# Kernel optimization log

Measured on AMD Instinct MI355X. Metric: run time of the kernel, lower is better.

Reference implementation:

```python
import jax, jax.numpy as jnp
import numpy as np

H, QP, VP, D, DP = 4, 4, 4, 128, 64
DH = D // H


def setup_inputs() -> dict:
    key = jax.random.key(0)
    ks = jax.random.split(key, 16)
    B, L = 1, 1024
    w_c0 = float(np.log(np.e - 1.0))
    inp = {
        'single': jax.random.normal(ks[0], (B, L, D), jnp.float32),
        'pair': jax.random.normal(ks[1], (B, L, L, DP), jnp.float32),
        'T': jax.random.normal(ks[2], (B, L, 4, 4), jnp.float32),
        'w_C': jnp.full((H,), w_c0, jnp.float32),
        'ln_g': jnp.ones((D,), jnp.float32),
        'ln_b': jnp.zeros((D,), jnp.float32),
        'Wq': jax.random.normal(ks[3], (D, H * DH), jnp.float32) * 0.05,
        'Wk': jax.random.normal(ks[4], (D, H * DH), jnp.float32) * 0.05,
        'Wv': jax.random.normal(ks[5], (D, H * DH), jnp.float32) * 0.05,
        'Wqpt': jax.random.normal(ks[6], (D, H * QP * 3), jnp.float32) * 0.05,
        'Wkpt': jax.random.normal(ks[7], (D, H * QP * 3), jnp.float32) * 0.05,
        'Wvpt': jax.random.normal(ks[8], (D, H * VP * 3), jnp.float32) * 0.05,
        'Wb': jax.random.normal(ks[9], (DP, H), jnp.float32) * 0.05,
        'Wout': jax.random.normal(ks[10], (H * (DH + DP + VP * 3 + VP), D), jnp.float32) * 0.05,
        'b_out': jnp.zeros((D,), jnp.float32),
    }
    return inp


def _layernorm(x, g, b, eps=1e-5):
    x32 = x.astype(jnp.float32)
    mu = x32.mean(-1, keepdims=True)
    var = ((x32 - mu) ** 2).mean(-1, keepdims=True)
    return ((x32 - mu) * jax.lax.rsqrt(var + eps) * g + b).astype(x.dtype)


def reference(single, pair, T, w_C, ln_g, ln_b, Wq, Wk, Wv, Wqpt, Wkpt, Wvpt, Wb, Wout, b_out):
    B, L, Dm = single.shape
    scale_attn = DH ** (-0.5)
    z = _layernorm(single, ln_g, ln_b)
    Q = (z @ Wq).reshape(B, L, H, DH)
    K = (z @ Wk).reshape(B, L, H, DH)
    V = (z @ Wv).reshape(B, L, H, DH)
    Q_pt = (z @ Wqpt).reshape(B, L, H, QP, 3)
    K_pt = (z @ Wkpt).reshape(B, L, H, QP, 3)
    V_pt = (z @ Wvpt).reshape(B, L, H, VP, 3)
    R = T[..., :3, :3]   # [B,L,3,3]
    t = T[..., :3, 3]    # [B,L,3]
    # global-frame points: R @ p + t
    Q_g = jnp.einsum('blxy,blhpy->blhpx', R, Q_pt) + t[:, :, None, None, :]
    K_g = jnp.einsum('blxy,blhpy->blhpx', R, K_pt) + t[:, :, None, None, :]
    V_g = jnp.einsum('blxy,blhpy->blhpx', R, V_pt) + t[:, :, None, None, :]
    # scalar QK score [B,H,L,L]
    s_attn = jnp.einsum('bihd,bjhd->bhij', Q, K) * scale_attn
    # pair bias [B,H,L,L]
    b_attn = jnp.einsum('bijc,ch->bhij', pair, Wb)
    # squared point distance [B,H,L,L]
    diff = Q_g[:, :, None] - K_g[:, None]          # [B,L,L,H,QP,3]
    d2 = jnp.moveaxis((diff ** 2).sum((-1, -2)), -1, 1)
    w_pt = jax.nn.softplus(w_C)[None, :, None, None]
    attn = jax.nn.softmax(s_attn + b_attn - 0.5 * w_pt * d2, axis=-1)
    # scalar values [B,L,H*DH]
    o_s = jnp.einsum('bhij,bjhd->bihd', attn, V).reshape(B, L, H * DH)
    # point values aggregated in global frame then mapped back: R^T (p - t)
    o_pt_g = jnp.einsum('bhij,bjhpx->bihpx', attn, V_g)
    o_pt = jnp.einsum('blyx,blhpy->blhpx', R, o_pt_g - t[:, :, None, None, :])
    o_pt_n = jnp.sqrt((o_pt ** 2).sum(-1))
    # pair aggregation [B,L,H*DP]
    o_pair = jnp.einsum('bhij,bijc->bihc', attn, pair).reshape(B, L, H * DP)
    out = jnp.concatenate([o_s, o_pair, o_pt.reshape(B, L, -1), o_pt_n.reshape(B, L, -1)], axis=-1)
    return single + out @ Wout + b_out
```

## Files before the change

kernel.cpp:

```cpp
#include <hip/hip_runtime.h>
#include <math.h>

#define L_SEQ 1024
#define DM 128
#define JC 64
#define NCHUNK (L_SEQ / JC)

#define OFF_KHAT 0
#define OFF_QHAT (L_SEQ * 192)
#define OFF_V    (OFF_QHAT + L_SEQ * 192)
#define OFF_VG   (OFF_V + L_SEQ * DM)

__global__ __launch_bounds__(256) void ipa_prep(
    const float* __restrict__ single, const float* __restrict__ T,
    const float* __restrict__ w_C, const float* __restrict__ ln_g, const float* __restrict__ ln_b,
    const float* __restrict__ Wq, const float* __restrict__ Wk, const float* __restrict__ Wv,
    const float* __restrict__ Wqpt, const float* __restrict__ Wkpt, const float* __restrict__ Wvpt,
    float* __restrict__ ws)
{
    __shared__ float z_lds[4][128];
    __shared__ float proj[4][528];
    __shared__ float qg[4][4][4][3];
    __shared__ float kg[4][4][4][3];
    __shared__ float cq[4][4], ck[4][4];

    const int t = threadIdx.x;
    const int wv = t >> 6, lane = t & 63;
    const int i0 = blockIdx.x << 2;
    const int i = i0 + wv;

    float x0 = single[i*DM + lane];
    float x1 = single[i*DM + 64 + lane];
    float s = x0 + x1, s2 = x0*x0 + x1*x1;
    #pragma unroll
    for (int off = 1; off < 64; off <<= 1) { s += __shfl_xor(s, off); s2 += __shfl_xor(s2, off); }
    float mu = s * 0.0078125f;
    float var = s2 * 0.0078125f - mu*mu;
    float rs = rsqrtf(var + 1e-5f);
    z_lds[wv][lane]      = (x0 - mu) * rs * ln_g[lane]      + ln_b[lane];
    z_lds[wv][lane + 64] = (x1 - mu) * rs * ln_g[lane + 64] + ln_b[lane + 64];
    __syncthreads();

    for (int cc = t; cc < 528; cc += 256) {
        const float* W; int col, ncol;
        if (cc < 128)      { W = Wq;   col = cc;       ncol = 128; }
        else if (cc < 256) { W = Wk;   col = cc - 128; ncol = 128; }
        else if (cc < 384) { W = Wv;   col = cc - 256; ncol = 128; }
        else if (cc < 432) { W = Wqpt; col = cc - 384; ncol = 48;  }
        else if (cc < 480) { W = Wkpt; col = cc - 432; ncol = 48;  }
        else               { W = Wvpt; col = cc - 480; ncol = 48;  }
        float a0 = 0.f, a1 = 0.f, a2 = 0.f, a3 = 0.f;
        #pragma unroll 8
        for (int k = 0; k < 128; ++k) {
            float w = W[k*ncol + col];
            a0 = fmaf(z_lds[0][k], w, a0);
            a1 = fmaf(z_lds[1][k], w, a1);
            a2 = fmaf(z_lds[2][k], w, a2);
            a3 = fmaf(z_lds[3][k], w, a3);
        }
        proj[0][cc] = a0; proj[1][cc] = a1; proj[2][cc] = a2; proj[3][cc] = a3;
    }
    __syncthreads();

    if (t < 64) {
        int r = t >> 4, h = (t >> 2) & 3, p = t & 3;
        int ii = i0 + r;
        float R[3][3], tt[3];
        #pragma unroll
        for (int x = 0; x < 3; ++x) {
            #pragma unroll
            for (int y = 0; y < 3; ++y) R[x][y] = T[ii*16 + x*4 + y];
            tt[x] = T[ii*16 + x*4 + 3];
        }
        int base = 384 + (h*4 + p)*3;
        float q0 = proj[r][base],    q1 = proj[r][base+1],  q2 = proj[r][base+2];
        float k0 = proj[r][base+48], k1 = proj[r][base+49], k2 = proj[r][base+50];
        float v0 = proj[r][base+96], v1 = proj[r][base+97], v2 = proj[r][base+98];
        #pragma unroll
        for (int x = 0; x < 3; ++x) {
            float qq = R[x][0]*q0 + R[x][1]*q1 + R[x][2]*q2 + tt[x];
            float kk = R[x][0]*k0 + R[x][1]*k1 + R[x][2]*k2 + tt[x];
            float vv = R[x][0]*v0 + R[x][1]*v1 + R[x][2]*v2 + tt[x];
            qg[r][h][p][x] = qq;
            kg[r][h][p][x] = kk;
            ws[OFF_VG + ii*48 + h*12 + p*3 + x] = vv;
        }
    }
    __syncthreads();

    if (t < 32) {
        int r = t >> 3, h = (t >> 1) & 3, isk = t & 1;
        float w = w_C[h];
        float wp = log1pf(__expf(w));
        float sq = 0.f;
        #pragma unroll
        for (int p = 0; p < 4; ++p)
            #pragma unroll
            for (int x = 0; x < 3; ++x) {
                float g = isk ? kg[r][h][p][x] : qg[r][h][p][x];
                sq += g*g;
            }
        float c = -0.5f * wp * sq;
        if (isk) ck[r][h] = c; else cq[r][h] = c;
    }
    __syncthreads();

    for (int idx = t; idx < 512; idx += 256) {
        int r = idx >> 7, d = idx & 127;
        ws[OFF_V + (size_t)(i0 + r)*DM + d] = proj[r][256 + d];
    }
    const float scale_attn = 0.17677669529663687f;
    for (int idx = t; idx < 768; idx += 256) {
        int r = idx / 192, rem = idx % 192;
        int h = rem / 48, k = rem % 48;
        int ii = i0 + r;
        float w = w_C[h];
        float wp = log1pf(__expf(w));
        float kv, qv;
        if (k < 32) {
            kv = proj[r][128 + h*32 + k];
            qv = scale_attn * proj[r][h*32 + k];
        } else if (k < 44) {
            int e = k - 32;
            kv = kg[r][h][e/3][e%3];
            qv = wp * qg[r][h][e/3][e%3];
        } else if (k == 44) { kv = ck[r][h]; qv = 1.0f; }
        else if (k == 45)   { kv = 1.0f;    qv = cq[r][h]; }
        else                { kv = 0.f;     qv = 0.f; }
        ws[OFF_KHAT + (size_t)ii*192 + h*48 + k] = kv;
        ws[OFF_QHAT + (size_t)ii*192 + h*48 + k] = qv;
    }
}

__global__ __launch_bounds__(256, 2) void ipa_attn(
    const float* __restrict__ single, const float* __restrict__ pair,
    const float* __restrict__ T, const float* __restrict__ Wb,
    const float* __restrict__ Wout, const float* __restrict__ b_out,
    const float* __restrict__ ws, float* __restrict__ out)
{
    __shared__ __align__(16) float4 pair_lds[2][JC][16];
    __shared__ float bias_part[4][2][JC][5];
    __shared__ float p_lds[4][2][JC];
    __shared__ float alpha_lds[4][2];
    __shared__ float l_lds[4][2];
    __shared__ __align__(16) float4 qhat_lds[2][4][12];
    __shared__ __align__(16) float4 wb_lds[64];
    __shared__ float og_lds[2][4][12];
    __shared__ __align__(16) float u_lds[2][448];

    const int t = threadIdx.x;
    const int wv = t >> 6, lane = t & 63;
    const int i0 = blockIdx.x * 2;

    if (t < 96)       ((float4*)qhat_lds)[t] = ((const float4*)(ws + OFF_QHAT))[(size_t)i0*48 + t];
    else if (t < 160) wb_lds[t - 96] = ((const float4*)Wb)[t - 96];

    float m0 = -INFINITY, m1 = -INFINITY, l0 = 0.f, l1 = 0.f;
    float4 accp[2][4];
    float4 accs[2];
    float4 accg[2];
    #pragma unroll
    for (int r = 0; r < 2; ++r) {
        accs[r] = make_float4(0.f,0.f,0.f,0.f);
        accg[r] = make_float4(0.f,0.f,0.f,0.f);
        #pragma unroll
        for (int h = 0; h < 4; ++h) accp[r][h] = make_float4(0.f,0.f,0.f,0.f);
    }

    const float4* pair4 = (const float4*)pair;
    const float4* kh4   = (const float4*)(ws + OFF_KHAT);
    const float4* v4    = (const float4*)(ws + OFF_V);
    const float4* vg4   = (const float4*)(ws + OFF_VG);

    __syncthreads();

    for (int ch = 0; ch < NCHUNK; ++ch) {
        const int j0 = ch * JC;
        #pragma unroll
        for (int it = 0; it < 8; ++it) {
            int idx = t + 256*it;
            int c4 = idx & 15, rj = idx >> 4;
            int row = rj >> 6, j = rj & 63;
            float4 pv = pair4[((size_t)(i0 + row)*L_SEQ + j0 + j)*16 + c4];
            pair_lds[row][j][c4 ^ (j & 7)] = pv;
        }
        __syncthreads();

        {
            float b00=0,b01=0,b02=0,b03=0, b10=0,b11=0,b12=0,b13=0;
            #pragma unroll
            for (int c4p = 0; c4p < 4; ++c4p) {
                int c4 = (wv << 2) + c4p;
                float4 w0 = wb_lds[c4*4+0], w1 = wb_lds[c4*4+1], w2 = wb_lds[c4*4+2], w3 = wb_lds[c4*4+3];
                int sw = c4 ^ (lane & 7);
                float4 p0 = pair_lds[0][lane][sw];
                float4 p1 = pair_lds[1][lane][sw];
                b00 += p0.x*w0.x + p0.y*w1.x + p0.z*w2.x + p0.w*w3.x;
                b01 += p0.x*w0.y + p0.y*w1.y + p0.z*w2.y + p0.w*w3.y;
                b02 += p0.x*w0.z + p0.y*w1.z + p0.z*w2.z + p0.w*w3.z;
                b03 += p0.x*w0.w + p0.y*w1.w + p0.z*w2.w + p0.w*w3.w;
                b10 += p1.x*w0.x + p1.y*w1.x + p1.z*w2.x + p1.w*w3.x;
                b11 += p1.x*w0.y + p1.y*w1.y + p1.z*w2.y + p1.w*w3.y;
                b12 += p1.x*w0.z + p1.y*w1.z + p1.z*w2.z + p1.w*w3.z;
                b13 += p1.x*w0.w + p1.y*w1.w + p1.z*w2.w + p1.w*w3.w;
            }
            bias_part[wv][0][lane][0]=b00; bias_part[wv][0][lane][1]=b01;
            bias_part[wv][0][lane][2]=b02; bias_part[wv][0][lane][3]=b03;
            bias_part[wv][1][lane][0]=b10; bias_part[wv][1][lane][1]=b11;
            bias_part[wv][1][lane][2]=b12; bias_part[wv][1][lane][3]=b13;
        }
        __syncthreads();

        {
            float4 kh[12];
            const float4* kp = kh4 + (size_t)(j0 + lane)*48 + wv*12;
            #pragma unroll
            for (int k4 = 0; k4 < 12; ++k4) kh[k4] = kp[k4];
            #pragma unroll
            for (int row = 0; row < 2; ++row) {
                float d = 0.f;
                #pragma unroll
                for (int k4 = 0; k4 < 12; ++k4) {
                    float4 q = qhat_lds[row][wv][k4];
                    d = fmaf(kh[k4].x, q.x, d); d = fmaf(kh[k4].y, q.y, d);
                    d = fmaf(kh[k4].z, q.z, d); d = fmaf(kh[k4].w, q.w, d);
                }
                float bias = bias_part[0][row][lane][wv] + bias_part[1][row][lane][wv]
                           + bias_part[2][row][lane][wv] + bias_part[3][row][lane][wv];
                float logit = d + bias;
                float cmax = logit;
                #pragma unroll
                for (int off = 1; off < 64; off <<= 1) cmax = fmaxf(cmax, __shfl_xor(cmax, off));
                float mo = row ? m1 : m0;
                float mn = fmaxf(mo, cmax);
                float alpha = __expf(mo - mn);
                float p = __expf(logit - mn);
                float ps = p;
                #pragma unroll
                for (int off = 1; off < 64; off <<= 1) ps += __shfl_xor(ps, off);
                if (row) { l1 = l1*alpha + ps; m1 = mn; } else { l0 = l0*alpha + ps; m0 = mn; }
                p_lds[wv][row][lane] = p;
                if (lane == 0) alpha_lds[wv][row] = alpha;
            }
        }
        __syncthreads();

        {
            float al[4][2];
            #pragma unroll
            for (int h = 0; h < 4; ++h) { al[h][0] = alpha_lds[h][0]; al[h][1] = alpha_lds[h][1]; }
            #pragma unroll
            for (int r = 0; r < 2; ++r) {
                #pragma unroll
                for (int h = 0; h < 4; ++h) {
                    float a = al[h][r];
                    accp[r][h].x *= a; accp[r][h].y *= a; accp[r][h].z *= a; accp[r][h].w *= a;
                }
                float a = al[wv][r];
                accs[r].x *= a; accs[r].y *= a; accs[r].z *= a; accs[r].w *= a;
                accg[r].x *= a; accg[r].y *= a; accg[r].z *= a; accg[r].w *= a;
            }
            {
                int c4p = lane & 3, jg = lane >> 2;
                #pragma unroll
                for (int jj = 0; jj < 4; ++jj) {
                    int j = jg + 16*jj;
                    int sw = ((wv << 2) + c4p) ^ (j & 7);
                    #pragma unroll
                    for (int r = 0; r < 2; ++r) {
                        float4 pv = pair_lds[r][j][sw];
                        float pw0 = p_lds[0][r][j], pw1 = p_lds[1][r][j];
                        float pw2 = p_lds[2][r][j], pw3 = p_lds[3][r][j];
                        accp[r][0].x = fmaf(pw0, pv.x, accp[r][0].x); accp[r][0].y = fmaf(pw0, pv.y, accp[r][0].y);
                        accp[r][0].z = fmaf(pw0, pv.z, accp[r][0].z); accp[r][0].w = fmaf(pw0, pv.w, accp[r][0].w);
                        accp[r][1].x = fmaf(pw1, pv.x, accp[r][1].x); accp[r][1].y = fmaf(pw1, pv.y, accp[r][1].y);
                        accp[r][1].z = fmaf(pw1, pv.z, accp[r][1].z); accp[r][1].w = fmaf(pw1, pv.w, accp[r][1].w);
                        accp[r][2].x = fmaf(pw2, pv.x, accp[r][2].x); accp[r][2].y = fmaf(pw2, pv.y, accp[r][2].y);
                        accp[r][2].z = fmaf(pw2, pv.z, accp[r][2].z); accp[r][2].w = fmaf(pw2, pv.w, accp[r][2].w);
                        accp[r][3].x = fmaf(pw3, pv.x, accp[r][3].x); accp[r][3].y = fmaf(pw3, pv.y, accp[r][3].y);
                        accp[r][3].z = fmaf(pw3, pv.z, accp[r][3].z); accp[r][3].w = fmaf(pw3, pv.w, accp[r][3].w);
                    }
                }
            }
            {
                int d4 = lane & 7, jg = lane >> 3;
                #pragma unroll
                for (int jj = 0; jj < 8; ++jj) {
                    int j = jg + 8*jj;
                    float4 vv = v4[(size_t)(j0 + j)*32 + wv*8 + d4];
                    float pa = p_lds[wv][0][j], pb = p_lds[wv][1][j];
                    accs[0].x = fmaf(pa, vv.x, accs[0].x); accs[0].y = fmaf(pa, vv.y, accs[0].y);
                    accs[0].z = fmaf(pa, vv.z, accs[0].z); accs[0].w = fmaf(pa, vv.w, accs[0].w);
                    accs[1].x = fmaf(pb, vv.x, accs[1].x); accs[1].y = fmaf(pb, vv.y, accs[1].y);
                    accs[1].z = fmaf(pb, vv.z, accs[1].z); accs[1].w = fmaf(pb, vv.w, accs[1].w);
                }
            }
            {
                int g4 = lane & 3, jg = lane >> 2;
                #pragma unroll
                for (int jj = 0; jj < 4; ++jj) {
                    int j = jg + 16*jj;
                    float4 gv = make_float4(0.f,0.f,0.f,0.f);
                    if (g4 < 3) gv = vg4[(size_t)(j0 + j)*12 + wv*3 + g4];
                    float pa = p_lds[wv][0][j], pb = p_lds[wv][1][j];
                    accg[0].x = fmaf(pa, gv.x, accg[0].x); accg[0].y = fmaf(pa, gv.y, accg[0].y);
                    accg[0].z = fmaf(pa, gv.z, accg[0].z); accg[0].w = fmaf(pa, gv.w, accg[0].w);
                    accg[1].x = fmaf(pb, gv.x, accg[1].x); accg[1].y = fmaf(pb, gv.y, accg[1].y);
                    accg[1].z = fmaf(pb, gv.z, accg[1].z); accg[1].w = fmaf(pb, gv.w, accg[1].w);
                }
            }
        }
        __syncthreads();
    }

    #pragma unroll
    for (int r = 0; r < 2; ++r) {
        #pragma unroll
        for (int h = 0; h < 4; ++h) {
            #pragma unroll
            for (int off = 4; off < 64; off <<= 1) {
                accp[r][h].x += __shfl_xor(accp[r][h].x, off);
                accp[r][h].y += __shfl_xor(accp[r][h].y, off);
                accp[r][h].z += __shfl_xor(accp[r][h].z, off);
                accp[r][h].w += __shfl_xor(accp[r][h].w, off);
            }
        }
        #pragma unroll
        for (int off = 8; off < 64; off <<= 1) {
            accs[r].x += __shfl_xor(accs[r].x, off); accs[r].y += __shfl_xor(accs[r].y, off);
            accs[r].z += __shfl_xor(accs[r].z, off); accs[r].w += __shfl_xor(accs[r].w, off);
        }
        #pragma unroll
        for (int off = 4; off < 64; off <<= 1) {
            accg[r].x += __shfl_xor(accg[r].x, off); accg[r].y += __shfl_xor(accg[r].y, off);
            accg[r].z += __shfl_xor(accg[r].z, off); accg[r].w += __shfl_xor(accg[r].w, off);
        }
    }
    if (lane == 0) { l_lds[wv][0] = l0; l_lds[wv][1] = l1; }
    __syncthreads();
    float invl[4][2];
    #pragma unroll
    for (int h = 0; h < 4; ++h) { invl[h][0] = 1.f / l_lds[h][0]; invl[h][1] = 1.f / l_lds[h][1]; }

    if (lane < 8) {
        #pragma unroll
        for (int r = 0; r < 2; ++r) {
            float sc = invl[wv][r];
            int base = wv*32 + lane*4;
            u_lds[r][base+0] = accs[r].x*sc; u_lds[r][base+1] = accs[r].y*sc;
            u_lds[r][base+2] = accs[r].z*sc; u_lds[r][base+3] = accs[r].w*sc;
        }
    }
    if (lane < 4) {
        #pragma unroll
        for (int r = 0; r < 2; ++r)
            #pragma unroll
            for (int h = 0; h < 4; ++h) {
                float sc = invl[h][r];
                int base = 128 + h*64 + wv*16 + lane*4;
                u_lds[r][base+0] = accp[r][h].x*sc; u_lds[r][base+1] = accp[r][h].y*sc;
                u_lds[r][base+2] = accp[r][h].z*sc; u_lds[r][base+3] = accp[r][h].w*sc;
            }
    }
    if (lane < 3) {
        #pragma unroll
        for (int r = 0; r < 2; ++r) {
            float sc = invl[wv][r];
            og_lds[r][wv][lane*4+0] = accg[r].x*sc; og_lds[r][wv][lane*4+1] = accg[r].y*sc;
            og_lds[r][wv][lane*4+2] = accg[r].z*sc; og_lds[r][wv][lane*4+3] = accg[r].w*sc;
        }
    }
    __syncthreads();

    if (t < 32) {
        int r = t >> 4, idx = t & 15, h = idx >> 2, p = idx & 3;
        int ii = i0 + r;
        float R[3][3], tt[3];
        #pragma unroll
        for (int x = 0; x < 3; ++x) {
            #pragma unroll
            for (int y = 0; y < 3; ++y) R[x][y] = T[ii*16 + x*4 + y];
            tt[x] = T[ii*16 + x*4 + 3];
        }
        float v0 = og_lds[r][h][p*3+0] - tt[0];
        float v1 = og_lds[r][h][p*3+1] - tt[1];
        float v2 = og_lds[r][h][p*3+2] - tt[2];
        float n2 = 0.f;
        #pragma unroll
        for (int x = 0; x < 3; ++x) {
            float o = R[0][x]*v0 + R[1][x]*v1 + R[2][x]*v2;
            u_lds[r][384 + h*12 + p*3 + x] = o;
            n2 += o*o;
        }
        u_lds[r][432 + h*4 + p] = sqrtf(n2);
    }
    __syncthreads();

    {
        int r = t >> 7, d = t & 127;
        int ii = i0 + r;
        float acc = single[ii*DM + d] + b_out[d];
        const float4* u4 = (const float4*)u_lds[r];
        #pragma unroll 4
        for (int k4 = 0; k4 < 112; ++k4) {
            float4 u = u4[k4];
            const float* wp = Wout + (size_t)(k4*4)*128 + d;
            acc = fmaf(u.x, wp[0],   acc);
            acc = fmaf(u.y, wp[128], acc);
            acc = fmaf(u.z, wp[256], acc);
            acc = fmaf(u.w, wp[384], acc);
        }
        out[ii*DM + d] = acc;
    }
}

extern "C" void kernel_launch(void* const* d_in, const int* in_sizes, int n_in,
                              void* d_out, int out_size, void* d_ws, size_t ws_size,
                              hipStream_t stream)
{
    const float* single = (const float*)d_in[0];
    const float* pair   = (const float*)d_in[1];
    const float* T      = (const float*)d_in[2];
    const float* w_C    = (const float*)d_in[3];
    const float* ln_g   = (const float*)d_in[4];
    const float* ln_b   = (const float*)d_in[5];
    const float* Wq     = (const float*)d_in[6];
    const float* Wk     = (const float*)d_in[7];
    const float* Wv     = (const float*)d_in[8];
    const float* Wqpt   = (const float*)d_in[9];
    const float* Wkpt   = (const float*)d_in[10];
    const float* Wvpt   = (const float*)d_in[11];
    const float* Wb     = (const float*)d_in[12];
    const float* Wout   = (const float*)d_in[13];
    const float* b_out  = (const float*)d_in[14];
    float* out = (float*)d_out;
    float* ws  = (float*)d_ws;

    ipa_prep<<<256, 256, 0, stream>>>(single, T, w_C, ln_g, ln_b, Wq, Wk, Wv, Wqpt, Wkpt, Wvpt, ws);
    ipa_attn<<<512, 256, 0, stream>>>(single, pair, T, Wb, Wout, b_out, ws, out);
}
```

Baseline: 494.4 us.

## Double-buffer pair tiles with async global-to-LDS loads and halve chunk size

Pair tiles are now loaded straight into LDS with global_load_lds into a two-slot buffer, so the next chunk's fetch overlaps compute on the current one. The chunk size drops from 64 to 32 keys, and each wave now handles both query rows at once with a remapped lane layout for the bias, softmax and accumulation stages. K-hat, V and VG loads are hoisted ahead of the bias stage to hide their latency. In exchange there are twice as many chunk iterations, barriers written in inline asm with hand-set vmcnt waits, and different reduction lane patterns that must match exactly.

Measured after the change: 473.8 us. 4.2% less time.

```diff
diff --git a/kernel.cpp b/kernel.cpp
--- a/kernel.cpp
+++ b/kernel.cpp
@@ -3,13 +3,21 @@
 
 #define L_SEQ 1024
 #define DM 128
-#define JC 64
-#define NCHUNK (L_SEQ / JC)
+#define JC 32
+#define NCH (L_SEQ / JC)
 
 #define OFF_KHAT 0
 #define OFF_QHAT (L_SEQ * 192)
 #define OFF_V    (OFF_QHAT + L_SEQ * 192)
 #define OFF_VG   (OFF_V + L_SEQ * DM)
+
+typedef __attribute__((address_space(1))) const void* gas_t;
+typedef __attribute__((address_space(3))) void* las_t;
+
+__device__ __forceinline__ void async16(const float4* g, float4* l) {
+    __builtin_amdgcn_global_load_lds((gas_t)g, (las_t)l, 16, 0, 0);
+}
+#define ASYNC_BAR() asm volatile("s_waitcnt lgkmcnt(0)\n\ts_barrier" ::: "memory")
 
 __global__ __launch_bounds__(256) void ipa_prep(
     const float* __restrict__ single, const float* __restrict__ T,
@@ -138,7 +146,7 @@
     const float* __restrict__ Wout, const float* __restrict__ b_out,
     const float* __restrict__ ws, float* __restrict__ out)
 {
-    __shared__ __align__(16) float4 pair_lds[2][JC][16];
+    __shared__ __align__(16) float4 pair_lds[2][2][JC][16];
     __shared__ float bias_part[4][2][JC][5];
     __shared__ float p_lds[4][2][JC];
     __shared__ float alpha_lds[4][2];
@@ -155,7 +163,14 @@
     if (t < 96)       ((float4*)qhat_lds)[t] = ((const float4*)(ws + OFF_QHAT))[(size_t)i0*48 + t];
     else if (t < 160) wb_lds[t - 96] = ((const float4*)Wb)[t - 96];
 
-    float m0 = -INFINITY, m1 = -INFINITY, l0 = 0.f, l1 = 0.f;
+    const int r_b = lane >> 5, j_b = lane & 31;
+    const int r_s = lane & 1,  j_s = lane >> 1;
+    const int d4  = lane & 7,  jg_s = lane >> 3;
+    const int c4p = lane >> 4, jg_p = lane & 15;
+    const int g4  = lane & 3,  jg_g = lane >> 2;
+    const int g4c = (g4 < 3) ? g4 : 0;
+
+    float m_run = -INFINITY, l_run = 0.f;
     float4 accp[2][4];
     float4 accs[2];
     float4 accg[2];
@@ -171,79 +186,98 @@
     const float4* kh4   = (const float4*)(ws + OFF_KHAT);
     const float4* v4    = (const float4*)(ws + OFF_V);
     const float4* vg4   = (const float4*)(ws + OFF_VG);
-
-    __syncthreads();
-
-    for (int ch = 0; ch < NCHUNK; ++ch) {
+    float4* plds_flat   = &pair_lds[0][0][0][0];
+
+    {
+        #pragma unroll
+        for (int it = 0; it < 4; ++it) {
+            int idx = it*256 + t;
+            int row = idx >> 9, j = (idx >> 4) & 31, slot = idx & 15;
+            int c4 = slot ^ (j & 7);
+            async16(pair4 + ((size_t)(i0 + row)*L_SEQ + j)*16 + c4, plds_flat + idx);
+        }
+    }
+
+    for (int ch = 0; ch < NCH; ++ch) {
+        const int cur = ch & 1;
         const int j0 = ch * JC;
-        #pragma unroll
-        for (int it = 0; it < 8; ++it) {
-            int idx = t + 256*it;
-            int c4 = idx & 15, rj = idx >> 4;
-            int row = rj >> 6, j = rj & 63;
-            float4 pv = pair4[((size_t)(i0 + row)*L_SEQ + j0 + j)*16 + c4];
-            pair_lds[row][j][c4 ^ (j & 7)] = pv;
-        }
-        __syncthreads();
-
+
+        ASYNC_BAR();
+        if (ch + 1 < NCH) {
+            const int jn = (ch + 1) * JC;
+            #pragma unroll
+            for (int it = 0; it < 4; ++it) {
+                int idx = it*256 + t;
+                int row = idx >> 9, j = (idx >> 4) & 31, slot = idx & 15;
+                int c4 = slot ^ (j & 7);
+                async16(pair4 + ((size_t)(i0 + row)*L_SEQ + jn + j)*16 + c4,
+                        plds_flat + (1 - cur)*1024 + idx);
+            }
+            asm volatile("s_waitcnt vmcnt(4)" ::: "memory");
+        } else {
+            asm volatile("s_waitcnt vmcnt(0)" ::: "memory");
+        }
+        ASYNC_BAR();
+
+        float4 kh[12];
         {
-            float b00=0,b01=0,b02=0,b03=0, b10=0,b11=0,b12=0,b13=0;
-            #pragma unroll
-            for (int c4p = 0; c4p < 4; ++c4p) {
-                int c4 = (wv << 2) + c4p;
+            const float4* kp = kh4 + (size_t)(j0 + j_s)*48 + wv*12;
+            #pragma unroll
+            for (int k4 = 0; k4 < 12; ++k4) kh[k4] = kp[k4];
+        }
+        float4 vv[4];
+        #pragma unroll
+        for (int jj = 0; jj < 4; ++jj)
+            vv[jj] = v4[(size_t)(j0 + jg_s + 8*jj)*32 + wv*8 + d4];
+        float4 gvv[2];
+        #pragma unroll
+        for (int jj = 0; jj < 2; ++jj)
+            gvv[jj] = vg4[(size_t)(j0 + jg_g + 16*jj)*12 + wv*3 + g4c];
+
+        {
+            float bx=0.f, by=0.f, bz=0.f, bw=0.f;
+            #pragma unroll
+            for (int cp = 0; cp < 4; ++cp) {
+                int c4 = (wv << 2) + cp;
+                int sw = c4 ^ (j_b & 7);
+                float4 pv = pair_lds[cur][r_b][j_b][sw];
                 float4 w0 = wb_lds[c4*4+0], w1 = wb_lds[c4*4+1], w2 = wb_lds[c4*4+2], w3 = wb_lds[c4*4+3];
-                int sw = c4 ^ (lane & 7);
-                float4 p0 = pair_lds[0][lane][sw];
-                float4 p1 = pair_lds[1][lane][sw];
-                b00 += p0.x*w0.x + p0.y*w1.x + p0.z*w2.x + p0.w*w3.x;
-                b01 += p0.x*w0.y + p0.y*w1.y + p0.z*w2.y + p0.w*w3.y;
-                b02 += p0.x*w0.z + p0.y*w1.z + p0.z*w2.z + p0.w*w3.z;
-                b03 += p0.x*w0.w + p0.y*w1.w + p0.z*w2.w + p0.w*w3.w;
-                b10 += p1.x*w0.x + p1.y*w1.x + p1.z*w2.x + p1.w*w3.x;
-                b11 += p1.x*w0.y + p1.y*w1.y + p1.z*w2.y + p1.w*w3.y;
-                b12 += p1.x*w0.z + p1.y*w1.z + p1.z*w2.z + p1.w*w3.z;
-                b13 += p1.x*w0.w + p1.y*w1.w + p1.z*w2.w + p1.w*w3.w;
-            }
-            bias_part[wv][0][lane][0]=b00; bias_part[wv][0][lane][1]=b01;
-            bias_part[wv][0][lane][2]=b02; bias_part[wv][0][lane][3]=b03;
-            bias_part[wv][1][lane][0]=b10; bias_part[wv][1][lane][1]=b11;
-            bias_part[wv][1][lane][2]=b12; bias_part[wv][1][lane][3]=b13;
-        }
-        __syncthreads();
+                bx += pv.x*w0.x + pv.y*w1.x + pv.z*w2.x + pv.w*w3.x;
+                by += pv.x*w0.y + pv.y*w1.y + pv.z*w2.y + pv.w*w3.y;
+                bz += pv.x*w0.z + pv.y*w1.z + pv.z*w2.z + pv.w*w3.z;
+                bw += pv.x*w0.w + pv.y*w1.w + pv.z*w2.w + pv.w*w3.w;
+            }
+            bias_part[wv][r_b][j_b][0] = bx; bias_part[wv][r_b][j_b][1] = by;
+            bias_part[wv][r_b][j_b][2] = bz; bias_part[wv][r_b][j_b][3] = bw;
+        }
+        ASYNC_BAR();
 
         {
-            float4 kh[12];
-            const float4* kp = kh4 + (size_t)(j0 + lane)*48 + wv*12;
-            #pragma unroll
-            for (int k4 = 0; k4 < 12; ++k4) kh[k4] = kp[k4];
-            #pragma unroll
-            for (int row = 0; row < 2; ++row) {
-                float d = 0.f;
-                #pragma unroll
-                for (int k4 = 0; k4 < 12; ++k4) {
-                    float4 q = qhat_lds[row][wv][k4];
-                    d = fmaf(kh[k4].x, q.x, d); d = fmaf(kh[k4].y, q.y, d);
-                    d = fmaf(kh[k4].z, q.z, d); d = fmaf(kh[k4].w, q.w, d);
-                }
-                float bias = bias_part[0][row][lane][wv] + bias_part[1][row][lane][wv]
-                           + bias_part[2][row][lane][wv] + bias_part[3][row][lane][wv];
-                float logit = d + bias;
-                float cmax = logit;
-                #pragma unroll
-                for (int off = 1; off < 64; off <<= 1) cmax = fmaxf(cmax, __shfl_xor(cmax, off));
-                float mo = row ? m1 : m0;
-                float mn = fmaxf(mo, cmax);
-                float alpha = __expf(mo - mn);
-                float p = __expf(logit - mn);
-                float ps = p;
-                #pragma unroll
-                for (int off = 1; off < 64; off <<= 1) ps += __shfl_xor(ps, off);
-                if (row) { l1 = l1*alpha + ps; m1 = mn; } else { l0 = l0*alpha + ps; m0 = mn; }
-                p_lds[wv][row][lane] = p;
-                if (lane == 0) alpha_lds[wv][row] = alpha;
-            }
-        }
-        __syncthreads();
+            float d = 0.f;
+            #pragma unroll
+            for (int k4 = 0; k4 < 12; ++k4) {
+                float4 q = qhat_lds[r_s][wv][k4];
+                d = fmaf(kh[k4].x, q.x, d); d = fmaf(kh[k4].y, q.y, d);
+                d = fmaf(kh[k4].z, q.z, d); d = fmaf(kh[k4].w, q.w, d);
+            }
+            float bias = bias_part[0][r_s][j_s][wv] + bias_part[1][r_s][j_s][wv]
+                       + bias_part[2][r_s][j_s][wv] + bias_part[3][r_s][j_s][wv];
+            float logit = d + bias;
+            float cmax = logit;
+            #pragma unroll
+            for (int off = 2; off < 64; off <<= 1) cmax = fmaxf(cmax, __shfl_xor(cmax, off));
+            float mn = fmaxf(m_run, cmax);
+            float alpha = __expf(m_run - mn);
+            float p = __expf(logit - mn);
+            float ps = p;
+            #pragma unroll
+            for (int off = 2; off < 64; off <<= 1) ps += __shfl_xor(ps, off);
+            l_run = l_run * alpha + ps;
+            m_run = mn;
+            p_lds[wv][r_s][j_s] = p;
+            if (j_s == 0) alpha_lds[wv][r_s] = alpha;
+        }
+        ASYNC_BAR();
 
         {
             float al[4][2];
@@ -260,57 +294,44 @@
                 accs[r].x *= a; accs[r].y *= a; accs[r].z *= a; accs[r].w *= a;
                 accg[r].x *= a; accg[r].y *= a; accg[r].z *= a; accg[r].w *= a;
             }
-            {
-                int c4p = lane & 3, jg = lane >> 2;
+            #pragma unroll
+            for (int jj = 0; jj < 2; ++jj) {
+                int j = jg_p + 16*jj;
+                int sw = ((wv << 2) + c4p) ^ (j & 7);
                 #pragma unroll
-                for (int jj = 0; jj < 4; ++jj) {
-                    int j = jg + 16*jj;
-                    int sw = ((wv << 2) + c4p) ^ (j & 7);
-                    #pragma unroll
-                    for (int r = 0; r < 2; ++r) {
-                        float4 pv = pair_lds[r][j][sw];
-                        float pw0 = p_lds[0][r][j], pw1 = p_lds[1][r][j];
-                        float pw2 = p_lds[2][r][j], pw3 = p_lds[3][r][j];
-                        accp[r][0].x = fmaf(pw0, pv.x, accp[r][0].x); accp[r][0].y = fmaf(pw0, pv.y, accp[r][0].y);
-                        accp[r][0].z = fmaf(pw0, pv.z, accp[r][0].z); accp[r][0].w = fmaf(pw0, pv.w, accp[r][0].w);
-                        accp[r][1].x = fmaf(pw1, pv.x, accp[r][1].x); accp[r][1].y = fmaf(pw1, pv.y, accp[r][1].y);
-                        accp[r][1].z = fmaf(pw1, pv.z, accp[r][1].z); accp[r][1].w = fmaf(pw1, pv.w, accp[r][1].w);
-                        accp[r][2].x = fmaf(pw2, pv.x, accp[r][2].x); accp[r][2].y = fmaf(pw2, pv.y, accp[r][2].y);
-                        accp[r][2].z = fmaf(pw2, pv.z, accp[r][2].z); accp[r][2].w = fmaf(pw2, pv.w, accp[r][2].w);
-                        accp[r][3].x = fmaf(pw3, pv.x, accp[r][3].x); accp[r][3].y = fmaf(pw3, pv.y, accp[r][3].y);
-                        accp[r][3].z = fmaf(pw3, pv.z, accp[r][3].z); accp[r][3].w = fmaf(pw3, pv.w, accp[r][3].w);
-                    }
+                for (int r = 0; r < 2; ++r) {
+                    float4 pv = pair_lds[cur][r][j][sw];
+                    float p0 = p_lds[0][r][j], p1 = p_lds[1][r][j];
+                    float p2 = p_lds[2][r][j], p3 = p_lds[3][r][j];
+                    accp[r][0].x = fmaf(p0, pv.x, accp[r][0].x); accp[r][0].y = fmaf(p0, pv.y, accp[r][0].y);
+                    accp[r][0].z = fmaf(p0, pv.z, accp[r][0].z); accp[r][0].w = fmaf(p0, pv.w, accp[r][0].w);
+                    accp[r][1].x = fmaf(p1, pv.x, accp[r][1].x); accp[r][1].y = fmaf(p1, pv.y, accp[r][1].y);
+                    accp[r][1].z = fmaf(p1, pv.z, accp[r][1].z); accp[r][1].w = fmaf(p1, pv.w, accp[r][1].w);
+                    accp[r][2].x = fmaf(p2, pv.x, accp[r][2].x); accp[r][2].y = fmaf(p2, pv.y, accp[r][2].y);
+                    accp[r][2].z = fmaf(p2, pv.z, accp[r][2].z); accp[r][2].w = fmaf(p2, pv.w, accp[r][2].w);
+                    accp[r][3].x = fmaf(p3, pv.x, accp[r][3].x); accp[r][3].y = fmaf(p3, pv.y, accp[r][3].y);
+                    accp[r][3].z = fmaf(p3, pv.z, accp[r][3].z); accp[r][3].w = fmaf(p3, pv.w, accp[r][3].w);
                 }
             }
-            {
-                int d4 = lane & 7, jg = lane >> 3;
-                #pragma unroll
-                for (int jj = 0; jj < 8; ++jj) {
-                    int j = jg + 8*jj;
-                    float4 vv = v4[(size_t)(j0 + j)*32 + wv*8 + d4];
-                    float pa = p_lds[wv][0][j], pb = p_lds[wv][1][j];
-                    accs[0].x = fmaf(pa, vv.x, accs[0].x); accs[0].y = fmaf(pa, vv.y, accs[0].y);
-                    accs[0].z = fmaf(pa, vv.z, accs[0].z); accs[0].w = fmaf(pa, vv.w, accs[0].w);
-                    accs[1].x = fmaf(pb, vv.x, accs[1].x); accs[1].y = fmaf(pb, vv.y, accs[1].y);
-                    accs[1].z = fmaf(pb, vv.z, accs[1].z); accs[1].w = fmaf(pb, vv.w, accs[1].w);
-                }
-            }
-            {
-                int g4 = lane & 3, jg = lane >> 2;
-                #pragma unroll
-                for (int jj = 0; jj < 4; ++jj) {
-                    int j = jg + 16*jj;
-                    float4 gv = make_float4(0.f,0.f,0.f,0.f);
-                    if (g4 < 3) gv = vg4[(size_t)(j0 + j)*12 + wv*3 + g4];
-                    float pa = p_lds[wv][0][j], pb = p_lds[wv][1][j];
-                    accg[0].x = fmaf(pa, gv.x, accg[0].x); accg[0].y = fmaf(pa, gv.y, accg[0].y);
-                    accg[0].z = fmaf(pa, gv.z, accg[0].z); accg[0].w = fmaf(pa, gv.w, accg[0].w);
-                    accg[1].x = fmaf(pb, gv.x, accg[1].x); accg[1].y = fmaf(pb, gv.y, accg[1].y);
-                    accg[1].z = fmaf(pb, gv.z, accg[1].z); accg[1].w = fmaf(pb, gv.w, accg[1].w);
-                }
-            }
-        }
-        __syncthreads();
+            #pragma unroll
+            for (int jj = 0; jj < 4; ++jj) {
+                int j = jg_s + 8*jj;
+                float pa = p_lds[wv][0][j], pb = p_lds[wv][1][j];
+                accs[0].x = fmaf(pa, vv[jj].x, accs[0].x); accs[0].y = fmaf(pa, vv[jj].y, accs[0].y);
+                accs[0].z = fmaf(pa, vv[jj].z, accs[0].z); accs[0].w = fmaf(pa, vv[jj].w, accs[0].w);
+                accs[1].x = fmaf(pb, vv[jj].x, accs[1].x); accs[1].y = fmaf(pb, vv[jj].y, accs[1].y);
+                accs[1].z = fmaf(pb, vv[jj].z, accs[1].z); accs[1].w = fmaf(pb, vv[jj].w, accs[1].w);
+            }
+            #pragma unroll
+            for (int jj = 0; jj < 2; ++jj) {
+                int j = jg_g + 16*jj;
+                float pa = p_lds[wv][0][j], pb = p_lds[wv][1][j];
+                accg[0].x = fmaf(pa, gvv[jj].x, accg[0].x); accg[0].y = fmaf(pa, gvv[jj].y, accg[0].y);
+                accg[0].z = fmaf(pa, gvv[jj].z, accg[0].z); accg[0].w = fmaf(pa, gvv[jj].w, accg[0].w);
+                accg[1].x = fmaf(pb, gvv[jj].x, accg[1].x); accg[1].y = fmaf(pb, gvv[jj].y, accg[1].y);
+                accg[1].z = fmaf(pb, gvv[jj].z, accg[1].z); accg[1].w = fmaf(pb, gvv[jj].w, accg[1].w);
+            }
+        }
     }
 
     #pragma unroll
@@ -318,7 +339,7 @@
         #pragma unroll
         for (int h = 0; h < 4; ++h) {
             #pragma unroll
-            for (int off = 4; off < 64; off <<= 1) {
+            for (int off = 1; off < 16; off <<= 1) {
                 accp[r][h].x += __shfl_xor(accp[r][h].x, off);
                 accp[r][h].y += __shfl_xor(accp[r][h].y, off);
                 accp[r][h].z += __shfl_xor(accp[r][h].z, off);
@@ -336,7 +357,7 @@
             accg[r].z += __shfl_xor(accg[r].z, off); accg[r].w += __shfl_xor(accg[r].w, off);
         }
     }
-    if (lane == 0) { l_lds[wv][0] = l0; l_lds[wv][1] = l1; }
+    if (lane < 2) l_lds[wv][lane] = l_run;
     __syncthreads();
     float invl[4][2];
     #pragma unroll
@@ -351,13 +372,14 @@
             u_lds[r][base+2] = accs[r].z*sc; u_lds[r][base+3] = accs[r].w*sc;
         }
     }
-    if (lane < 4) {
+    if ((lane & 15) == 0) {
+        int c4 = wv*4 + (lane >> 4);
         #pragma unroll
         for (int r = 0; r < 2; ++r)
             #pragma unroll
             for (int h = 0; h < 4; ++h) {
                 float sc = invl[h][r];
-                int base = 128 + h*64 + wv*16 + lane*4;
+                int base = 128 + h*64 + c4*4;
                 u_lds[r][base+0] = accp[r][h].x*sc; u_lds[r][base+1] = accp[r][h].y*sc;
                 u_lds[r][base+2] = accp[r][h].z*sc; u_lds[r][base+3] = accp[r][h].w*sc;
             }
```
